# Performance work log

Hardware: AMD Instinct MI355X
Metric: run time of the kernel (lower is better)

## Reference

```python
import jax, jax.numpy as jnp
import numpy as np
from jax import lax

D_MODEL, D_INNER, D_STATE, D_CONV, DT_RANK, N_LAYERS = 768, 1536, 16, 4, 48, 2
EPS = 1e-5


def rmsnorm(h, w):
    var = jnp.mean(jnp.square(h), axis=-1, keepdims=True)
    return h * lax.rsqrt(var + EPS) * w


def mamba_mixer(h, in_w, cw, cb, xp_w, dtp_w, dtp_b, A_log, Dp, out_w):
    B, L, _ = h.shape
    xz = jnp.einsum('bld,ed->ble', h, in_w)            # [B,L,2*Di]
    xc, z = jnp.split(xz, 2, axis=-1)
    # causal depthwise conv over time
    xc_t = xc.transpose(0, 2, 1)                        # [B,Di,L]
    xc_t = lax.conv_general_dilated(
        xc_t, cw[:, None, :], window_strides=(1,),
        padding=[(D_CONV - 1, 0)], feature_group_count=D_INNER)
    xc = jax.nn.silu(xc_t + cb[None, :, None]).transpose(0, 2, 1)  # [B,L,Di]
    # input-dependent dt, B, C
    x_dbl = jnp.einsum('bld,ed->ble', xc, xp_w)         # [B,L,dtr+2*ds]
    dt, Bm, Cm = jnp.split(x_dbl, [DT_RANK, DT_RANK + D_STATE], axis=-1)
    delta = jax.nn.softplus(jnp.einsum('blr,dr->bld', dt, dtp_w) + dtp_b)
    A = -jnp.exp(A_log)                                 # [Di,ds]
    deltaA = jnp.exp(jnp.einsum('bld,dn->bldn', delta, A))
    dBu = jnp.einsum('bld,bln,bld->bldn', delta, Bm, xc)

    def step(s, inp):
        dA_t, dBu_t, C_t = inp                          # [B,Di,ds],[B,Di,ds],[B,ds]
        s = dA_t * s + dBu_t
        y = jnp.einsum('bdn,bn->bd', s, C_t)
        return s, y

    s0 = jnp.zeros((B, D_INNER, D_STATE), h.dtype)
    _, ys = lax.scan(step, s0, (deltaA.transpose(1, 0, 2, 3),
                                dBu.transpose(1, 0, 2, 3),
                                Cm.transpose(1, 0, 2)))
    y = ys.transpose(1, 0, 2) + xc * Dp                 # [B,L,Di]
    y = y * jax.nn.silu(z)
    return jnp.einsum('ble,de->bld', y, out_w)          # [B,L,D]


def reference(x, in_proj_w, conv_w, conv_b, x_proj_w, dt_proj_w, dt_proj_b,
              A_log, D_param, out_proj_w, norm_w, final_norm_w):
    h = x
    for i in range(N_LAYERS):
        h = h + mamba_mixer(rmsnorm(h, norm_w[i]), in_proj_w[i], conv_w[i],
                            conv_b[i], x_proj_w[i], dt_proj_w[i], dt_proj_b[i],
                            A_log[i], D_param[i], out_proj_w[i])
    h = rmsnorm(h, final_norm_w)
    return h[:, -1, :]                                  # last-token embedding [B,D]


def setup_inputs() -> dict:
    key = jax.random.key(0)
    ks = jax.random.split(key, 12)
    B, L = 2, 1024
    sc = lambda *s: 1.0 / np.sqrt(s[-1])
    return {
        'x': jax.random.normal(ks[0], (B, L, D_MODEL), jnp.float32),
        'in_proj_w': jax.random.normal(ks[1], (N_LAYERS, 2 * D_INNER, D_MODEL), jnp.float32) * sc(0, D_MODEL),
        'conv_w': jax.random.normal(ks[2], (N_LAYERS, D_INNER, D_CONV), jnp.float32) * sc(0, D_CONV),
        'conv_b': jax.random.normal(ks[3], (N_LAYERS, D_INNER), jnp.float32) * 0.02,
        'x_proj_w': jax.random.normal(ks[4], (N_LAYERS, DT_RANK + 2 * D_STATE, D_INNER), jnp.float32) * sc(0, D_INNER),
        'dt_proj_w': jax.random.normal(ks[5], (N_LAYERS, D_INNER, DT_RANK), jnp.float32) * sc(0, DT_RANK),
        'dt_proj_b': jax.random.normal(ks[6], (N_LAYERS, D_INNER), jnp.float32) * 0.02,
        'A_log': jnp.log(jnp.broadcast_to(jnp.arange(1, D_STATE + 1, dtype=jnp.float32), (N_LAYERS, D_INNER, D_STATE))),
        'D_param': jnp.ones((N_LAYERS, D_INNER), jnp.float32),
        'out_proj_w': jax.random.normal(ks[7], (N_LAYERS, D_MODEL, D_INNER), jnp.float32) * sc(0, D_INNER),
        'norm_w': jnp.ones((N_LAYERS, D_MODEL), jnp.float32),
        'final_norm_w': jnp.ones((D_MODEL,), jnp.float32),
    }
```

## Files before the change

kernel.cpp:

```cpp
#include <hip/hip_runtime.h>
#include <math.h>

#define NB 2
#define NL 1024
#define DM 768
#define DI 1536
#define DS 16
#define DCONV 4
#define DTR 48
#define NLAYERS 2
#define NTOK (NB*NL)

#define NCHUNK 32
#define SCHUNK 32

typedef unsigned short u16;
typedef __attribute__((ext_vector_type(8))) short bf16x8;
typedef __attribute__((ext_vector_type(4))) float f32x4;

__device__ __forceinline__ float softplus_f(float x) {
    return fmaxf(x, 0.f) + log1pf(expf(-fabsf(x)));
}
__device__ __forceinline__ u16 f2bf(float f) {
    union { float f; unsigned u; } x{f};
    unsigned r = x.u + 0x7fff + ((x.u >> 16) & 1);
    return (u16)(r >> 16);
}
__device__ __forceinline__ float bf2f(u16 u) {
    union { unsigned u; float f; } x{(unsigned)u << 16};
    return x.f;
}

__device__ __forceinline__ size_t pool_addr(int field, int b, int ch, int d, int n) {
    return (((size_t)(field * NB + b) * NCHUNK + ch) * DI + d) * DS + n;
}

#define CVT_N0 (NLAYERS*2*DI*DM/4)
#define CVT_N1 (NLAYERS*(DTR+2*DS)*DI/4)
#define CVT_N2 (NLAYERS*DM*DI/4)
__global__ __launch_bounds__(256)
void cvt_all_k(const float* __restrict__ in_w, const float* __restrict__ xp_w,
               const float* __restrict__ out_w,
               u16* __restrict__ win, u16* __restrict__ wxp, u16* __restrict__ wout)
{
    int i = blockIdx.x * 256 + threadIdx.x;
    const float* src; u16* dst; int j;
    if (i < CVT_N0)                 { src = in_w;  dst = win;  j = i; }
    else if (i < CVT_N0 + CVT_N1)   { src = xp_w;  dst = wxp;  j = i - CVT_N0; }
    else if (i < CVT_N0 + CVT_N1 + CVT_N2) { src = out_w; dst = wout; j = i - CVT_N0 - CVT_N1; }
    else return;
    float4 v = ((const float4*)src)[j];
    unsigned p0 = (unsigned)f2bf(v.x) | ((unsigned)f2bf(v.y) << 16);
    unsigned p1 = (unsigned)f2bf(v.z) | ((unsigned)f2bf(v.w) << 16);
    ((uint2*)dst)[j] = make_uint2(p0, p1);
}

__global__ __launch_bounds__(256)
void rmsnorm_k(const float* __restrict__ in, const float* __restrict__ w,
               u16* __restrict__ out)
{
    int t = blockIdx.x;
    int tid = threadIdx.x;
    const float* row = in + (size_t)t * DM;
    float v0 = row[tid], v1 = row[tid + 256], v2 = row[tid + 512];
    float ss = v0*v0 + v1*v1 + v2*v2;
    #pragma unroll
    for (int m = 32; m >= 1; m >>= 1) ss += __shfl_xor(ss, m, 64);
    __shared__ float red[4];
    if ((tid & 63) == 0) red[tid >> 6] = ss;
    __syncthreads();
    ss = red[0] + red[1] + red[2] + red[3];
    float sc = rsqrtf(ss * (1.f / DM) + 1e-5f);
    u16* orow = out + (size_t)t * DM;
    orow[tid]       = f2bf(v0 * sc * w[tid]);
    orow[tid + 256] = f2bf(v1 * sc * w[tid + 256]);
    orow[tid + 512] = f2bf(v2 * sc * w[tid + 512]);
}

__global__ __launch_bounds__(256)
void final_norm_k(const float* __restrict__ h, const float* __restrict__ w,
                  float* __restrict__ out)
{
    int b = blockIdx.x;
    int tid = threadIdx.x;
    const float* row = h + ((size_t)b * NL + (NL - 1)) * DM;
    float v0 = row[tid], v1 = row[tid + 256], v2 = row[tid + 512];
    float ss = v0*v0 + v1*v1 + v2*v2;
    #pragma unroll
    for (int m = 32; m >= 1; m >>= 1) ss += __shfl_xor(ss, m, 64);
    __shared__ float red[4];
    if ((tid & 63) == 0) red[tid >> 6] = ss;
    __syncthreads();
    ss = red[0] + red[1] + red[2] + red[3];
    float sc = rsqrtf(ss * (1.f / DM) + 1e-5f);
    float* orow = out + (size_t)b * DM;
    orow[tid]       = v0 * sc * w[tid];
    orow[tid + 256] = v1 * sc * w[tid + 256];
    orow[tid + 512] = v2 * sc * w[tid + 512];
}

template<int BM, int BN, int WM, int WN, int EPI>
__global__ __launch_bounds__(256)
void mfma_nt(const u16* __restrict__ A, const u16* __restrict__ B,
             void* __restrict__ Cv, const float* __restrict__ resid,
             int K, int ldc)
{
    constexpr int BK = 32;
    constexpr int MR = BM / WM / 16;
    constexpr int NR = BN / WN / 16;
    constexpr int ALOADS = BM / 16;
    constexpr int BLOADS = BN / 16;
    constexpr int NLOADS = ALOADS + BLOADS;

    __shared__ alignas(16) u16 lds[2][(BM + BN) * BK];

    const int tid  = threadIdx.x;
    const int lane = tid & 63;
    const int w    = tid >> 6;

    int nwg = gridDim.x * gridDim.y;
    int id  = blockIdx.y * gridDim.x + blockIdx.x;
    if ((nwg & 7) == 0) id = (id & 7) * (nwg >> 3) + (id >> 3);
    const int bm = (id / gridDim.x) * BM;
    const int bn = (id % gridDim.x) * BN;

    const int wm0  = (w / WN) * (BM / WM);
    const int wn0  = (w % WN) * (BN / WN);

    f32x4 acc[MR][NR] = {};

    const int lrow4 = lane >> 2;
    const int lslot = lane & 3;

    auto stage = [&](int buf, int k0) {
        #pragma unroll
        for (int idx = 0; idx < NLOADS; ++idx) {
            if ((idx & 3) != w) continue;
            const bool isA = idx < ALOADS;
            const int rowbase = (isA ? idx : idx - ALOADS) * 16;
            const int r = rowbase + lrow4;
            const int c = (lslot - (r >> 1)) & 3;
            const u16* src = (isA ? A + (size_t)(bm + r) * K
                                  : B + (size_t)(bn + r) * K) + k0 + c * 8;
            u16* dst = &lds[buf][((isA ? 0 : BM) + rowbase) * BK];
            __builtin_amdgcn_global_load_lds(
                (const __attribute__((address_space(1))) void*)src,
                (__attribute__((address_space(3))) void*)dst, 16, 0, 0);
        }
    };

    const int frow   = lane & 15;
    const int fchunk = lane >> 4;
    const int nk = K / BK;

    stage(0, 0);
    for (int kt = 0; kt < nk; ++kt) {
        __syncthreads();
        if (kt + 1 < nk) stage((kt + 1) & 1, (kt + 1) * BK);
        const int buf = kt & 1;
        bf16x8 a[MR], b[NR];
        #pragma unroll
        for (int i = 0; i < MR; ++i) {
            int row = wm0 + i * 16 + frow;
            int ch = (fchunk + (row >> 1)) & 3;
            a[i] = *(const bf16x8*)&lds[buf][row * BK + ch * 8];
        }
        #pragma unroll
        for (int j = 0; j < NR; ++j) {
            int row = wn0 + j * 16 + frow;
            int ch = (fchunk + (row >> 1)) & 3;
            b[j] = *(const bf16x8*)&lds[buf][(BM + row) * BK + ch * 8];
        }
        #pragma unroll
        for (int i = 0; i < MR; ++i)
            #pragma unroll
            for (int j = 0; j < NR; ++j)
                acc[i][j] = __builtin_amdgcn_mfma_f32_16x16x32_bf16(
                                a[i], b[j], acc[i][j], 0, 0, 0);
    }

    #pragma unroll
    for (int i = 0; i < MR; ++i) {
        #pragma unroll
        for (int j = 0; j < NR; ++j) {
            const int col  = bn + wn0 + j * 16 + (lane & 15);
            const int row0 = bm + wm0 + i * 16 + (lane >> 4) * 4;
            #pragma unroll
            for (int r = 0; r < 4; ++r) {
                float v = acc[i][j][r];
                size_t off = (size_t)(row0 + r) * ldc + col;
                if (EPI == 3) {
                    ((u16*)Cv)[off] = f2bf(v);
                } else {
                    if (EPI == 2) v += resid[off];
                    ((float*)Cv)[off] = v;
                }
            }
        }
    }
}

__global__ __launch_bounds__(384)
void conv_silu_k(const u16* __restrict__ xz, const float* __restrict__ cw,
                 const float* __restrict__ cb, u16* __restrict__ xconv)
{
    int t = blockIdx.x;
    int l = t & (NL - 1), b = t >> 10;
    int d0 = threadIdx.x * 4;

    float acc[4];
    {
        float4 cbv = *(const float4*)(cb + d0);
        acc[0] = cbv.x; acc[1] = cbv.y; acc[2] = cbv.z; acc[3] = cbv.w;
    }
    float wv[16];
    {
        const float4* cwp = (const float4*)(cw + (size_t)d0 * DCONV);
        *(float4*)&wv[0]  = cwp[0];
        *(float4*)&wv[4]  = cwp[1];
        *(float4*)&wv[8]  = cwp[2];
        *(float4*)&wv[12] = cwp[3];
    }
    #pragma unroll
    for (int k = 0; k < DCONV; ++k) {
        int ll = l - (DCONV - 1) + k;
        if (ll < 0) continue;
        ushort4 v = *(const ushort4*)(xz + (size_t)(b * NL + ll) * (2*DI) + d0);
        acc[0] = fmaf(bf2f(v.x), wv[0*4 + k], acc[0]);
        acc[1] = fmaf(bf2f(v.y), wv[1*4 + k], acc[1]);
        acc[2] = fmaf(bf2f(v.z), wv[2*4 + k], acc[2]);
        acc[3] = fmaf(bf2f(v.w), wv[3*4 + k], acc[3]);
    }
    ushort4 o;
    {
        float s0 = acc[0] / (1.f + __expf(-acc[0]));
        float s1 = acc[1] / (1.f + __expf(-acc[1]));
        float s2 = acc[2] / (1.f + __expf(-acc[2]));
        float s3 = acc[3] / (1.f + __expf(-acc[3]));
        o.x = f2bf(s0); o.y = f2bf(s1); o.z = f2bf(s2); o.w = f2bf(s3);
    }
    *(ushort4*)(xconv + (size_t)t * DI + d0) = o;
}

__global__ __launch_bounds__(256)
void gemm_sp_k(const float* __restrict__ A, const float* __restrict__ B,
               u16* __restrict__ C, int M, int N, int K, int lda, int ldb, int ldc,
               const float* __restrict__ bias)
{
    __shared__ __align__(16) float As[16][68];
    __shared__ __align__(16) float Bs[16][68];
    int tid = threadIdx.x;
    int tx = tid & 15, ty = tid >> 4;
    int bm = blockIdx.y * 64, bn = blockIdx.x * 64;
    float acc[4][4] = {};
    for (int k0 = 0; k0 < K; k0 += 16) {
        #pragma unroll
        for (int j = 0; j < 4; ++j) {
            As[tx][ty + 16*j] = A[(size_t)(bm + ty + 16*j) * lda + k0 + tx];
            Bs[tx][ty + 16*j] = B[(size_t)(bn + ty + 16*j) * ldb + k0 + tx];
        }
        __syncthreads();
        #pragma unroll
        for (int kk = 0; kk < 16; ++kk) {
            float4 av = *(const float4*)&As[kk][ty*4];
            float4 bv = *(const float4*)&Bs[kk][tx*4];
            float a[4] = {av.x, av.y, av.z, av.w};
            float b[4] = {bv.x, bv.y, bv.z, bv.w};
            #pragma unroll
            for (int i = 0; i < 4; ++i)
                #pragma unroll
                for (int j = 0; j < 4; ++j)
                    acc[i][j] = fmaf(a[i], b[j], acc[i][j]);
        }
        __syncthreads();
    }
    #pragma unroll
    for (int i = 0; i < 4; ++i) {
        int m = bm + ty*4 + i;
        int n = bn + tx*4;
        float vx = softplus_f(acc[i][0] + bias[n + 0]);
        float vy = softplus_f(acc[i][1] + bias[n + 1]);
        float vz = softplus_f(acc[i][2] + bias[n + 2]);
        float vw = softplus_f(acc[i][3] + bias[n + 3]);
        unsigned p0 = (unsigned)f2bf(vx) | ((unsigned)f2bf(vy) << 16);
        unsigned p1 = (unsigned)f2bf(vz) | ((unsigned)f2bf(vw) << 16);
        *(uint2*)(C + (size_t)m * ldc + n) = make_uint2(p0, p1);
    }
}

__global__ __launch_bounds__(64)
void scan_part_k(const u16* __restrict__ delta, const u16* __restrict__ xconv,
                 const float* __restrict__ xdbl, const float* __restrict__ A_log,
                 float* __restrict__ pool)
{
    int lane = threadIdx.x;
    int half = lane >> 5, c32 = lane & 31;
    int d = blockIdx.x * 32 + c32;
    int b = blockIdx.y, ch = blockIdx.z;
    int n0 = half * 8;
    int t0 = b * NL + ch * SCHUNK;

    __shared__ float bs[SCHUNK][16];
    for (int s = lane; s < SCHUNK * 4; s += 64) {
        int st = s >> 2, q = s & 3;
        *(float4*)&bs[st][q * 4] =
            *(const float4*)(xdbl + (size_t)(t0 + st) * 80 + 48 + q * 4);
    }
    __syncthreads();

    float a[8];
    {
        const float* al = A_log + (size_t)d * DS + n0;
        #pragma unroll
        for (int n = 0; n < 8; ++n) a[n] = -__expf(al[n]);
    }
    float s_[8];
    #pragma unroll
    for (int n = 0; n < 8; ++n) s_[n] = 0.f;
    float sdv = 0.f;

    float dvA[4], xcA[4], dvB[4], xcB[4];
    auto ld = [&](int j, float (&dv)[4], float (&xc)[4]) {
        #pragma unroll
        for (int k = 0; k < 4; ++k) {
            int t = t0 + j + k;
            dv[k] = bf2f(delta[(size_t)t * DI + d]);
            xc[k] = bf2f(xconv[(size_t)t * DI + d]);
        }
    };
    auto cp = [&](int j, float (&dv)[4], float (&xc)[4]) {
        #pragma unroll
        for (int k = 0; k < 4; ++k) {
            float u = dv[k] * xc[k];
            sdv += dv[k];
            float bb[8];
            *(float4*)&bb[0] = *(const float4*)&bs[j + k][n0];
            *(float4*)&bb[4] = *(const float4*)&bs[j + k][n0 + 4];
            #pragma unroll
            for (int n = 0; n < 8; ++n) {
                float e = __expf(dv[k] * a[n]);
                s_[n] = fmaf(e, s_[n], u * bb[n]);
            }
        }
    };
    ld(0, dvA, xcA);
    for (int j = 0; j < SCHUNK; j += 8) {
        ld(j + 4, dvB, xcB);
        cp(j, dvA, xcA);
        if (j + 8 < SCHUNK) ld(j + 8, dvA, xcA);
        cp(j + 4, dvB, xcB);
    }

    float pr[8];
    #pragma unroll
    for (int n = 0; n < 8; ++n) pr[n] = __expf(sdv * a[n]);

    size_t b0 = pool_addr(0, b, ch, d, n0);
    size_t b1 = pool_addr(1, b, ch, d, n0);
    *(float4*)(pool + b0)     = make_float4(pr[0], pr[1], pr[2], pr[3]);
    *(float4*)(pool + b0 + 4) = make_float4(pr[4], pr[5], pr[6], pr[7]);
    *(float4*)(pool + b1)     = make_float4(s_[0], s_[1], s_[2], s_[3]);
    *(float4*)(pool + b1 + 4) = make_float4(s_[4], s_[5], s_[6], s_[7]);
}

__global__ __launch_bounds__(256)
void scan_prefix_k(float* __restrict__ pool)
{
    int dn = blockIdx.x * 256 + threadIdx.x;
    int b = blockIdx.y;
    int d = dn >> 4, n = dn & 15;
    float run = 0.f;
    for (int g = 0; g < NCHUNK; g += 8) {
        float p[8], f[8];
        #pragma unroll
        for (int j = 0; j < 8; ++j) {
            p[j] = pool[pool_addr(0, b, g + j, d, n)];
            f[j] = pool[pool_addr(1, b, g + j, d, n)];
        }
        #pragma unroll
        for (int j = 0; j < 8; ++j) {
            pool[pool_addr(0, b, g + j, d, n)] = run;
            run = fmaf(p[j], run, f[j]);
        }
    }
}

__global__ __launch_bounds__(64)
void scan_emit_k(const u16* __restrict__ delta, const u16* __restrict__ xconv,
                 const u16* __restrict__ zin,
                 u16* __restrict__ yout,
                 const float* __restrict__ xdbl, const float* __restrict__ A_log,
                 const float* __restrict__ Dp, const float* __restrict__ pool)
{
    int lane = threadIdx.x;
    int half = lane >> 5, c32 = lane & 31;
    int d = blockIdx.x * 32 + c32;
    int b = blockIdx.y, ch = blockIdx.z;
    int n0 = half * 8;
    int t0 = b * NL + ch * SCHUNK;

    __shared__ float bcs[SCHUNK][32];
    for (int s = lane; s < SCHUNK * 8; s += 64) {
        int st = s >> 3, q = s & 7;
        *(float4*)&bcs[st][q * 4] =
            *(const float4*)(xdbl + (size_t)(t0 + st) * 80 + 48 + q * 4);
    }
    __syncthreads();

    float a[8];
    {
        const float* al = A_log + (size_t)d * DS + n0;
        #pragma unroll
        for (int n = 0; n < 8; ++n) a[n] = -__expf(al[n]);
    }
    float dpv = Dp[d];

    float s_[8];
    {
        size_t base = pool_addr(0, b, ch, d, n0);
        float4 v0 = *(const float4*)(pool + base);
        float4 v1 = *(const float4*)(pool + base + 4);
        s_[0]=v0.x; s_[1]=v0.y; s_[2]=v0.z; s_[3]=v0.w;
        s_[4]=v1.x; s_[5]=v1.y; s_[6]=v1.z; s_[7]=v1.w;
    }

    float dvA[4], xcA[4], zvA[4], dvB[4], xcB[4], zvB[4];
    auto ld = [&](int j, float (&dv)[4], float (&xc)[4], float (&zv)[4]) {
        #pragma unroll
        for (int k = 0; k < 4; ++k) {
            int t = t0 + j + k;
            dv[k] = bf2f(delta[(size_t)t * DI + d]);
            xc[k] = bf2f(xconv[(size_t)t * DI + d]);
            zv[k] = bf2f(zin[(size_t)t * (2*DI) + d]);
        }
    };
    auto cp = [&](int j, float (&dv)[4], float (&xc)[4], float (&zv)[4]) {
        #pragma unroll
        for (int k = 0; k < 4; ++k) {
            float u = dv[k] * xc[k];
            float bb[8], cc[8];
            *(float4*)&bb[0] = *(const float4*)&bcs[j + k][n0];
            *(float4*)&bb[4] = *(const float4*)&bcs[j + k][n0 + 4];
            *(float4*)&cc[0] = *(const float4*)&bcs[j + k][16 + n0];
            *(float4*)&cc[4] = *(const float4*)&bcs[j + k][16 + n0 + 4];
            float y0 = 0.f;
            #pragma unroll
            for (int n = 0; n < 8; ++n) {
                float e = __expf(dv[k] * a[n]);
                s_[n] = fmaf(e, s_[n], u * bb[n]);
                y0 = fmaf(s_[n], cc[n], y0);
            }
            float p = y0 + __shfl_xor(y0, 32, 64);
            if (half == 0) {
                float zv_ = zv[k];
                float y = p + xc[k] * dpv;
                y = y * zv_ / (1.f + __expf(-zv_));
                yout[(size_t)(t0 + j + k) * DI + d] = f2bf(y);
            }
        }
    };
    ld(0, dvA, xcA, zvA);
    for (int j = 0; j < SCHUNK; j += 8) {
        ld(j + 4, dvB, xcB, zvB);
        cp(j, dvA, xcA, zvA);
        if (j + 8 < SCHUNK) ld(j + 8, dvA, xcA, zvA);
        cp(j + 4, dvB, xcB, zvB);
    }
}

extern "C" void kernel_launch(void* const* d_in, const int* in_sizes, int n_in,
                              void* d_out, int out_size, void* d_ws, size_t ws_size,
                              hipStream_t stream) {
    const float* x       = (const float*)d_in[0];
    const float* in_w    = (const float*)d_in[1];
    const float* conv_w  = (const float*)d_in[2];
    const float* conv_b  = (const float*)d_in[3];
    const float* xp_w    = (const float*)d_in[4];
    const float* dtp_w   = (const float*)d_in[5];
    const float* dtp_b   = (const float*)d_in[6];
    const float* A_log   = (const float*)d_in[7];
    const float* D_param = (const float*)d_in[8];
    const float* out_w   = (const float*)d_in[9];
    const float* norm_w  = (const float*)d_in[10];
    const float* fnorm_w = (const float*)d_in[11];
    float* out = (float*)d_out;

    float* ws     = (float*)d_ws;
    float* h      = ws;
    float* xdbl   = h + (size_t)NTOK * DM;
    float* pool   = xdbl + (size_t)NTOK * 80;
    u16*  xz      = (u16*)(pool + (size_t)2*NB*NCHUNK*DI*DS);
    u16*  hnb     = xz + (size_t)NTOK * 2 * DI;
    u16*  xcbf    = hnb + (size_t)NTOK * DM;
    u16*  ybf     = xcbf + (size_t)NTOK * DI;
    u16*  dyb     = ybf + (size_t)NTOK * DI;
    u16*  wbf_in  = dyb + (size_t)NTOK * DI;
    u16*  wbf_xp  = wbf_in + (size_t)NLAYERS * 2*DI*DM;
    u16*  wbf_out = wbf_xp + (size_t)NLAYERS * 80*DI;

    cvt_all_k<<<(CVT_N0 + CVT_N1 + CVT_N2 + 255) / 256, 256, 0, stream>>>(
        in_w, xp_w, out_w, wbf_in, wbf_xp, wbf_out);

    for (int layer = 0; layer < NLAYERS; ++layer) {
        const float* hin = (layer == 0) ? x : h;
        const float* Alog_l = A_log + (size_t)layer * DI * DS;
        const u16* win_l  = wbf_in  + (size_t)layer * 2*DI*DM;
        const u16* wxp_l  = wbf_xp  + (size_t)layer * 80*DI;
        const u16* wout_l = wbf_out + (size_t)layer * DM*DI;

        rmsnorm_k<<<NTOK, 256, 0, stream>>>(hin, norm_w + layer * DM, hnb);

        mfma_nt<128, 128, 2, 2, 3><<<dim3((2*DI)/128, NTOK/128), 256, 0, stream>>>(
            hnb, win_l, xz, nullptr, DM, 2*DI);

        conv_silu_k<<<NTOK, 384, 0, stream>>>(
            xz, conv_w + (size_t)layer * DI * DCONV, conv_b + (size_t)layer * DI, xcbf);

        mfma_nt<64, 80, 4, 1, 0><<<dim3(1, NTOK/64), 256, 0, stream>>>(
            xcbf, wxp_l, xdbl, nullptr, DI, 80);

        gemm_sp_k<<<dim3(DI/64, NTOK/64), 256, 0, stream>>>(
            xdbl, dtp_w + (size_t)layer * DI * DTR, dyb,
            NTOK, DI, DTR, 80, DTR, DI, dtp_b + (size_t)layer * DI);

        scan_part_k<<<dim3(DI/32, NB, NCHUNK), 64, 0, stream>>>(
            dyb, xcbf, xdbl, Alog_l, pool);
        scan_prefix_k<<<dim3((DI*DS)/256, NB), 256, 0, stream>>>(pool);
        scan_emit_k<<<dim3(DI/32, NB, NCHUNK), 64, 0, stream>>>(
            dyb, xcbf, xz + DI, ybf, xdbl, Alog_l,
            D_param + (size_t)layer * DI, pool);

        mfma_nt<64, 128, 2, 2, 2><<<dim3(DM/128, NTOK/64), 256, 0, stream>>>(
            ybf, wout_l, h, hin, DI, DM);
    }

    final_norm_k<<<NB, 256, 0, stream>>>(h, fnorm_w, out);
}
```

Before: 282.4 us.

## Fuse conv+silu, x_proj and dt_proj+softplus into one per-token-block kernel

Replaces three kernels per layer (conv+silu, the MFMA x_proj GEMM, and the fp32 dt_proj GEMM with softplus) with one kernel that handles 8 tokens per block. The conv output stays in shared memory in fp32 and feeds a scalar-FMA x_proj dot product against bf16 weights. The dt part is kept in LDS for dt_proj, and only the B/C columns are written out to a narrower buffer. This removes two launches and the global round trips of xconv and xdbl, but the x_proj now runs on scalar FMAs rather than MFMA and rereads the x_proj weights in every block. That could make this stage compute-bound. The x_proj input also changes from bf16 to fp32 conv output, so numerics shift slightly.

```diff
diff --git a/kernel.cpp b/kernel.cpp
--- a/kernel.cpp
+++ b/kernel.cpp
@@ -13,6 +13,7 @@
 
 #define NCHUNK 32
 #define SCHUNK 32
+#define TB 8
 
 typedef unsigned short u16;
 typedef __attribute__((ext_vector_type(8))) short bf16x8;
@@ -200,97 +201,150 @@
     }
 }
 
-__global__ __launch_bounds__(384)
-void conv_silu_k(const u16* __restrict__ xz, const float* __restrict__ cw,
-                 const float* __restrict__ cb, u16* __restrict__ xconv)
-{
-    int t = blockIdx.x;
-    int l = t & (NL - 1), b = t >> 10;
-    int d0 = threadIdx.x * 4;
-
-    float acc[4];
-    {
-        float4 cbv = *(const float4*)(cb + d0);
-        acc[0] = cbv.x; acc[1] = cbv.y; acc[2] = cbv.z; acc[3] = cbv.w;
-    }
-    float wv[16];
-    {
-        const float4* cwp = (const float4*)(cw + (size_t)d0 * DCONV);
-        *(float4*)&wv[0]  = cwp[0];
-        *(float4*)&wv[4]  = cwp[1];
-        *(float4*)&wv[8]  = cwp[2];
-        *(float4*)&wv[12] = cwp[3];
-    }
+__global__ __launch_bounds__(256)
+void fused_mid_k(const u16* __restrict__ xz,
+                 const float* __restrict__ cw,
+                 const float* __restrict__ cb,
+                 const u16* __restrict__ wxp,
+                 const float* __restrict__ dtw,
+                 const float* __restrict__ dtb,
+                 u16* __restrict__ xconv,
+                 float* __restrict__ xbc,
+                 u16* __restrict__ ddelta)
+{
+    __shared__ float xcl[TB][DI + 4];
+    __shared__ float dtl[TB][DTR];
+    const int tid = threadIdx.x;
+    const int t0 = blockIdx.x * TB;
+    const int b = t0 >> 10, l0 = t0 & (NL - 1);
+
+    if (tid < 192) {
+        const int d0 = tid * 8;
+        float wv[8][4];
+        #pragma unroll
+        for (int c = 0; c < 8; ++c)
+            *(float4*)wv[c] = *(const float4*)(cw + (size_t)(d0 + c) * DCONV);
+        float cbv[8];
+        *(float4*)&cbv[0] = *(const float4*)(cb + d0);
+        *(float4*)&cbv[4] = *(const float4*)(cb + d0 + 4);
+
+        float xv[TB + 3][8];
+        #pragma unroll
+        for (int w = 0; w < TB + 3; ++w) {
+            int ll = l0 - 3 + w;
+            if (ll >= 0) {
+                const u16* p = xz + (size_t)(b * NL + ll) * (2*DI) + d0;
+                ushort4 v0 = *(const ushort4*)p;
+                ushort4 v1 = *(const ushort4*)(p + 4);
+                xv[w][0] = bf2f(v0.x); xv[w][1] = bf2f(v0.y);
+                xv[w][2] = bf2f(v0.z); xv[w][3] = bf2f(v0.w);
+                xv[w][4] = bf2f(v1.x); xv[w][5] = bf2f(v1.y);
+                xv[w][6] = bf2f(v1.z); xv[w][7] = bf2f(v1.w);
+            } else {
+                #pragma unroll
+                for (int c = 0; c < 8; ++c) xv[w][c] = 0.f;
+            }
+        }
+        #pragma unroll
+        for (int j = 0; j < TB; ++j) {
+            float acc[8];
+            #pragma unroll
+            for (int c = 0; c < 8; ++c) acc[c] = cbv[c];
+            #pragma unroll
+            for (int k = 0; k < DCONV; ++k) {
+                #pragma unroll
+                for (int c = 0; c < 8; ++c)
+                    acc[c] = fmaf(xv[j + k][c], wv[c][k], acc[c]);
+            }
+            ushort4 o0, o1;
+            float s0 = acc[0] / (1.f + __expf(-acc[0]));
+            float s1 = acc[1] / (1.f + __expf(-acc[1]));
+            float s2 = acc[2] / (1.f + __expf(-acc[2]));
+            float s3 = acc[3] / (1.f + __expf(-acc[3]));
+            float s4 = acc[4] / (1.f + __expf(-acc[4]));
+            float s5 = acc[5] / (1.f + __expf(-acc[5]));
+            float s6 = acc[6] / (1.f + __expf(-acc[6]));
+            float s7 = acc[7] / (1.f + __expf(-acc[7]));
+            *(float4*)&xcl[j][d0]     = make_float4(s0, s1, s2, s3);
+            *(float4*)&xcl[j][d0 + 4] = make_float4(s4, s5, s6, s7);
+            o0.x = f2bf(s0); o0.y = f2bf(s1); o0.z = f2bf(s2); o0.w = f2bf(s3);
+            o1.x = f2bf(s4); o1.y = f2bf(s5); o1.z = f2bf(s6); o1.w = f2bf(s7);
+            u16* op = xconv + (size_t)(t0 + j) * DI + d0;
+            *(ushort4*)op = o0;
+            *(ushort4*)(op + 4) = o1;
+        }
+    }
+    __syncthreads();
+
     #pragma unroll
-    for (int k = 0; k < DCONV; ++k) {
-        int ll = l - (DCONV - 1) + k;
-        if (ll < 0) continue;
-        ushort4 v = *(const ushort4*)(xz + (size_t)(b * NL + ll) * (2*DI) + d0);
-        acc[0] = fmaf(bf2f(v.x), wv[0*4 + k], acc[0]);
-        acc[1] = fmaf(bf2f(v.y), wv[1*4 + k], acc[1]);
-        acc[2] = fmaf(bf2f(v.z), wv[2*4 + k], acc[2]);
-        acc[3] = fmaf(bf2f(v.w), wv[3*4 + k], acc[3]);
-    }
-    ushort4 o;
-    {
-        float s0 = acc[0] / (1.f + __expf(-acc[0]));
-        float s1 = acc[1] / (1.f + __expf(-acc[1]));
-        float s2 = acc[2] / (1.f + __expf(-acc[2]));
-        float s3 = acc[3] / (1.f + __expf(-acc[3]));
-        o.x = f2bf(s0); o.y = f2bf(s1); o.z = f2bf(s2); o.w = f2bf(s3);
-    }
-    *(ushort4*)(xconv + (size_t)t * DI + d0) = o;
-}
-
-__global__ __launch_bounds__(256)
-void gemm_sp_k(const float* __restrict__ A, const float* __restrict__ B,
-               u16* __restrict__ C, int M, int N, int K, int lda, int ldb, int ldc,
-               const float* __restrict__ bias)
-{
-    __shared__ __align__(16) float As[16][68];
-    __shared__ __align__(16) float Bs[16][68];
-    int tid = threadIdx.x;
-    int tx = tid & 15, ty = tid >> 4;
-    int bm = blockIdx.y * 64, bn = blockIdx.x * 64;
-    float acc[4][4] = {};
-    for (int k0 = 0; k0 < K; k0 += 16) {
-        #pragma unroll
-        for (int j = 0; j < 4; ++j) {
-            As[tx][ty + 16*j] = A[(size_t)(bm + ty + 16*j) * lda + k0 + tx];
-            Bs[tx][ty + 16*j] = B[(size_t)(bn + ty + 16*j) * ldb + k0 + tx];
-        }
-        __syncthreads();
-        #pragma unroll
-        for (int kk = 0; kk < 16; ++kk) {
-            float4 av = *(const float4*)&As[kk][ty*4];
-            float4 bv = *(const float4*)&Bs[kk][tx*4];
-            float a[4] = {av.x, av.y, av.z, av.w};
-            float b[4] = {bv.x, bv.y, bv.z, bv.w};
-            #pragma unroll
-            for (int i = 0; i < 4; ++i)
+    for (int r = 0; r < 3; ++r) {
+        int oid = tid + r * 256;
+        if (oid < TB * 80) {
+            int t = oid / 80, e = oid - t * 80;
+            const u16* wp = wxp + (size_t)e * DI;
+            float sum = 0.f;
+            for (int k = 0; k < DI; k += 8) {
+                bf16x8 wv8 = *(const bf16x8*)(wp + k);
+                float4 x0 = *(const float4*)&xcl[t][k];
+                float4 x1 = *(const float4*)&xcl[t][k + 4];
+                sum = fmaf(bf2f((u16)wv8[0]), x0.x, sum);
+                sum = fmaf(bf2f((u16)wv8[1]), x0.y, sum);
+                sum = fmaf(bf2f((u16)wv8[2]), x0.z, sum);
+                sum = fmaf(bf2f((u16)wv8[3]), x0.w, sum);
+                sum = fmaf(bf2f((u16)wv8[4]), x1.x, sum);
+                sum = fmaf(bf2f((u16)wv8[5]), x1.y, sum);
+                sum = fmaf(bf2f((u16)wv8[6]), x1.z, sum);
+                sum = fmaf(bf2f((u16)wv8[7]), x1.w, sum);
+            }
+            if (e < DTR) dtl[t][e] = sum;
+            else xbc[(size_t)(t0 + t) * 32 + (e - DTR)] = sum;
+        }
+    }
+    __syncthreads();
+
+    if (tid < 192) {
+        const int d0 = tid * 8;
+        float acc[TB][8] = {};
+        for (int k0 = 0; k0 < DTR; k0 += 4) {
+            float w4[8][4];
+            #pragma unroll
+            for (int c = 0; c < 8; ++c)
+                *(float4*)w4[c] = *(const float4*)(dtw + (size_t)(d0 + c) * DTR + k0);
+            #pragma unroll
+            for (int j = 0; j < TB; ++j) {
+                float dt4[4];
+                *(float4*)dt4 = *(const float4*)&dtl[j][k0];
                 #pragma unroll
-                for (int j = 0; j < 4; ++j)
-                    acc[i][j] = fmaf(a[i], b[j], acc[i][j]);
-        }
-        __syncthreads();
-    }
-    #pragma unroll
-    for (int i = 0; i < 4; ++i) {
-        int m = bm + ty*4 + i;
-        int n = bn + tx*4;
-        float vx = softplus_f(acc[i][0] + bias[n + 0]);
-        float vy = softplus_f(acc[i][1] + bias[n + 1]);
-        float vz = softplus_f(acc[i][2] + bias[n + 2]);
-        float vw = softplus_f(acc[i][3] + bias[n + 3]);
-        unsigned p0 = (unsigned)f2bf(vx) | ((unsigned)f2bf(vy) << 16);
-        unsigned p1 = (unsigned)f2bf(vz) | ((unsigned)f2bf(vw) << 16);
-        *(uint2*)(C + (size_t)m * ldc + n) = make_uint2(p0, p1);
+                for (int kk = 0; kk < 4; ++kk)
+                    #pragma unroll
+                    for (int c = 0; c < 8; ++c)
+                        acc[j][c] = fmaf(dt4[kk], w4[c][kk], acc[j][c]);
+            }
+        }
+        float bias[8];
+        *(float4*)&bias[0] = *(const float4*)(dtb + d0);
+        *(float4*)&bias[4] = *(const float4*)(dtb + d0 + 4);
+        #pragma unroll
+        for (int j = 0; j < TB; ++j) {
+            ushort4 o0, o1;
+            o0.x = f2bf(softplus_f(acc[j][0] + bias[0]));
+            o0.y = f2bf(softplus_f(acc[j][1] + bias[1]));
+            o0.z = f2bf(softplus_f(acc[j][2] + bias[2]));
+            o0.w = f2bf(softplus_f(acc[j][3] + bias[3]));
+            o1.x = f2bf(softplus_f(acc[j][4] + bias[4]));
+            o1.y = f2bf(softplus_f(acc[j][5] + bias[5]));
+            o1.z = f2bf(softplus_f(acc[j][6] + bias[6]));
+            o1.w = f2bf(softplus_f(acc[j][7] + bias[7]));
+            u16* op = ddelta + (size_t)(t0 + j) * DI + d0;
+            *(ushort4*)op = o0;
+            *(ushort4*)(op + 4) = o1;
+        }
     }
 }
 
 __global__ __launch_bounds__(64)
 void scan_part_k(const u16* __restrict__ delta, const u16* __restrict__ xconv,
-                 const float* __restrict__ xdbl, const float* __restrict__ A_log,
+                 const float* __restrict__ xbc, const float* __restrict__ A_log,
                  float* __restrict__ pool)
 {
     int lane = threadIdx.x;
@@ -304,7 +358,7 @@
     for (int s = lane; s < SCHUNK * 4; s += 64) {
         int st = s >> 2, q = s & 3;
         *(float4*)&bs[st][q * 4] =
-            *(const float4*)(xdbl + (size_t)(t0 + st) * 80 + 48 + q * 4);
+            *(const float4*)(xbc + (size_t)(t0 + st) * 32 + q * 4);
     }
     __syncthreads();
 
@@ -389,7 +443,7 @@
 void scan_emit_k(const u16* __restrict__ delta, const u16* __restrict__ xconv,
                  const u16* __restrict__ zin,
                  u16* __restrict__ yout,
-                 const float* __restrict__ xdbl, const float* __restrict__ A_log,
+                 const float* __restrict__ xbc, const float* __restrict__ A_log,
                  const float* __restrict__ Dp, const float* __restrict__ pool)
 {
     int lane = threadIdx.x;
@@ -403,7 +457,7 @@
     for (int s = lane; s < SCHUNK * 8; s += 64) {
         int st = s >> 3, q = s & 7;
         *(float4*)&bcs[st][q * 4] =
-            *(const float4*)(xdbl + (size_t)(t0 + st) * 80 + 48 + q * 4);
+            *(const float4*)(xbc + (size_t)(t0 + st) * 32 + q * 4);
     }
     __syncthreads();
 
@@ -487,8 +541,8 @@
 
     float* ws     = (float*)d_ws;
     float* h      = ws;
-    float* xdbl   = h + (size_t)NTOK * DM;
-    float* pool   = xdbl + (size_t)NTOK * 80;
+    float* xbc    = h + (size_t)NTOK * DM;
+    float* pool   = xbc + (size_t)NTOK * 32;
     u16*  xz      = (u16*)(pool + (size_t)2*NB*NCHUNK*DI*DS);
     u16*  hnb     = xz + (size_t)NTOK * 2 * DI;
     u16*  xcbf    = hnb + (size_t)NTOK * DM;
@@ -513,21 +567,16 @@
         mfma_nt<128, 128, 2, 2, 3><<<dim3((2*DI)/128, NTOK/128), 256, 0, stream>>>(
             hnb, win_l, xz, nullptr, DM, 2*DI);
 
-        conv_silu_k<<<NTOK, 384, 0, stream>>>(
-            xz, conv_w + (size_t)layer * DI * DCONV, conv_b + (size_t)layer * DI, xcbf);
-
-        mfma_nt<64, 80, 4, 1, 0><<<dim3(1, NTOK/64), 256, 0, stream>>>(
-            xcbf, wxp_l, xdbl, nullptr, DI, 80);
-
-        gemm_sp_k<<<dim3(DI/64, NTOK/64), 256, 0, stream>>>(
-            xdbl, dtp_w + (size_t)layer * DI * DTR, dyb,
-            NTOK, DI, DTR, 80, DTR, DI, dtp_b + (size_t)layer * DI);
+        fused_mid_k<<<NTOK/TB, 256, 0, stream>>>(
+            xz, conv_w + (size_t)layer * DI * DCONV, conv_b + (size_t)layer * DI,
+            wxp_l, dtp_w + (size_t)layer * DI * DTR, dtp_b + (size_t)layer * DI,
+            xcbf, xbc, dyb);
 
         scan_part_k<<<dim3(DI/32, NB, NCHUNK), 64, 0, stream>>>(
-            dyb, xcbf, xdbl, Alog_l, pool);
+            dyb, xcbf, xbc, Alog_l, pool);
         scan_prefix_k<<<dim3((DI*DS)/256, NB), 256, 0, stream>>>(pool);
         scan_emit_k<<<dim3(DI/32, NB, NCHUNK), 64, 0, stream>>>(
-            dyb, xcbf, xz + DI, ybf, xdbl, Alog_l,
+            dyb, xcbf, xz + DI, ybf, xbc, Alog_l,
             D_param + (size_t)layer * DI, pool);
 
         mfma_nt<64, 128, 2, 2, 2><<<dim3(DM/128, NTOK/64), 256, 0, stream>>>(
```

Result: slower. 472.7 us (+67.4%).
